# Kernel tuning notes

Hardware: AMD Instinct MI355X
Metric: run time of the kernel (lower is better)

The kernel has to match this reference:

```python
import jax, jax.numpy as jnp
import numpy as np

B, L, E, H = 2, 2048, 1024, 16
D = E // H

def setup_inputs() -> dict:
    key = jax.random.key(0)
    ks = jax.random.split(key, 6)
    values = jax.random.normal(ks[0], (B, L, E), dtype=jnp.float32)
    keys = jax.random.normal(ks[1], (B, L, E), dtype=jnp.float32)
    query = jax.random.normal(ks[2], (B, L, E), dtype=jnp.float32)
    mask = jax.random.randint(ks[3], (B, 1, L, L), 0, 2, dtype=jnp.int32)
    W_out = jax.random.normal(ks[4], (E, E), dtype=jnp.float32) * 0.02
    b_out = jax.random.normal(ks[5], (E,), dtype=jnp.float32) * 0.02
    return {"values": values, "keys": keys, "query": query, "mask": mask,
            "W_out": W_out, "b_out": b_out}

def reference(values, keys, query, mask, W_out, b_out):
    # Note: source module never applies its per-head q/k/v Linear layers;
    # it only reshapes inputs, so we do the same.
    b, l, e = query.shape
    v = values.reshape(b, l, H, D)   # [B, K, H, D]
    k = keys.reshape(b, l, H, D)     # [B, K, H, D]
    q = query.reshape(b, l, H, D)    # [B, Q, H, D]
    # scores[b,h,q,k] = sum_d q[b,q,h,d] * k[b,k,h,d]
    scores = jnp.einsum('bqhd,bkhd->bhqk', q, k)
    scores = jnp.where(mask == 0, jnp.float32(-1e20), scores)
    # source scales by 1/sqrt(embed_size), not head_dim
    attn = jax.nn.softmax(scores / jnp.float32(E ** 0.5), axis=3)
    out = jnp.einsum('bhqk,bkhd->bqhd', attn, v).reshape(b, l, e)
    out = out @ W_out.T + b_out  # torch Linear: x @ W^T + b
    return out
```

## Files before the change

### kernel.cpp

```cpp
#include <hip/hip_runtime.h>
#include <hip/hip_bf16.h>

typedef __bf16 bf16;
typedef __bf16 bf16x8 __attribute__((ext_vector_type(8)));
typedef __bf16 bf16x4 __attribute__((ext_vector_type(4)));
typedef float  f32x4  __attribute__((ext_vector_type(4)));

#define B_ 2
#define L_ 2048
#define E_ 1024
#define H_ 16
#define D_ 64

__device__ __forceinline__ int swz(int r, int c) {
    return r * 64 + (((c ^ (r & 7)) & 7) << 3);
}

__global__ __launch_bounds__(256) void cvt_bf16_kernel(const float* __restrict__ in,
                                                       bf16* __restrict__ out, int n4, float scale) {
    int i = blockIdx.x * blockDim.x + threadIdx.x;
    int stride = gridDim.x * blockDim.x;
    for (; i < n4; i += stride) {
        float4 f = reinterpret_cast<const float4*>(in)[i];
        bf16x4 o;
        o.x = (bf16)(f.x * scale); o.y = (bf16)(f.y * scale);
        o.z = (bf16)(f.z * scale); o.w = (bf16)(f.w * scale);
        reinterpret_cast<bf16x4*>(out)[i] = o;
    }
}

__global__ __launch_bounds__(256) void vtrans_kernel(const float* __restrict__ v,
                                                     bf16* __restrict__ vt) {
    __shared__ __attribute__((aligned(16))) bf16 tile[64 * 72];
    int bh = blockIdx.y;
    int b = bh >> 4, h = bh & 15;
    int k0 = blockIdx.x * 64;
    int t = threadIdx.x;
    int kk = t >> 2, d0 = (t & 3) * 16;
    const float* src = v + (((size_t)(b * L_ + k0 + kk)) * H_ + h) * D_ + d0;
    float4 f[4];
#pragma unroll
    for (int i = 0; i < 4; i++) f[i] = reinterpret_cast<const float4*>(src)[i];
#pragma unroll
    for (int i = 0; i < 16; i++) {
        float val = reinterpret_cast<const float*>(f)[i];
        tile[(d0 + i) * 72 + kk] = (bf16)val;
    }
    __syncthreads();
    int dd = t >> 2, c = (t & 3) * 16;
    bf16* dst = vt + ((size_t)bh * 64 + dd) * 2048 + k0 + c;
    *reinterpret_cast<uint4*>(dst)     = *reinterpret_cast<const uint4*>(&tile[dd * 72 + c]);
    *reinterpret_cast<uint4*>(dst + 8) = *reinterpret_cast<const uint4*>(&tile[dd * 72 + c + 8]);
}

__global__ __launch_bounds__(256) void mtrans_kernel(const int* __restrict__ mask,
                                                     unsigned short* __restrict__ mt) {
    __shared__ __attribute__((aligned(16))) unsigned char tile[64 * 80];
    int b = blockIdx.z;
    int q0 = blockIdx.x * 64, k0 = blockIdx.y * 64;
    int t = threadIdx.x;
    int qq = t >> 2, kc = (t & 3) * 16;
    const int* src = mask + (size_t)b * L_ * L_ + (size_t)(q0 + qq) * L_ + k0 + kc;
    int4 m[4];
#pragma unroll
    for (int i = 0; i < 4; i++) m[i] = reinterpret_cast<const int4*>(src)[i];
#pragma unroll
    for (int i = 0; i < 16; i++)
        tile[(kc + i) * 80 + qq] = (unsigned char)reinterpret_cast<const int*>(m)[i];
    __syncthreads();
    int kk = t >> 2, q16 = (t & 3) * 16;
    unsigned int v = 0;
#pragma unroll
    for (int i = 0; i < 16; i++)
        v |= ((unsigned int)(tile[kk * 80 + q16 + i] & 1)) << i;
    mt[((size_t)(b * L_) + k0 + kk) * (L_ / 16) + (q0 >> 4) + (t & 3)] = (unsigned short)v;
}

__global__ __launch_bounds__(256, 4) void attn_kernel(const bf16* __restrict__ qb,
                                                      const bf16* __restrict__ kb,
                                                      const bf16* __restrict__ vt,
                                                      const unsigned int* __restrict__ mt,
                                                      bf16* __restrict__ xb) {
    __shared__ __attribute__((aligned(16))) bf16 Qs[64 * 64];
    __shared__ __attribute__((aligned(16))) bf16 Ks[64 * 64];
    __shared__ __attribute__((aligned(16))) bf16 Vs[64 * 64];
    __shared__ __attribute__((aligned(16))) bf16 Ps[4][16 * 72];
    __shared__ unsigned int Ms32[64 * 2];

    const int bh = blockIdx.y, b = bh >> 4, h = bh & 15;
    const int q0 = blockIdx.x * 64;
    const int t = threadIdx.x;
    const int w = t >> 6, lane = t & 63, quad = lane >> 4, ln = lane & 15;
    const int r_ = t >> 2, c2 = (t & 3) * 2;

    {
        const bf16* src = qb + (((size_t)(b * L_ + q0 + r_)) * H_ + h) * D_ + c2 * 8;
        *reinterpret_cast<uint4*>(&Qs[swz(r_, c2)])     = *reinterpret_cast<const uint4*>(src);
        *reinterpret_cast<uint4*>(&Qs[swz(r_, c2 + 1)]) = *reinterpret_cast<const uint4*>(src + 8);
    }
    __syncthreads();

    bf16x8 aq[2];
#pragma unroll
    for (int dc = 0; dc < 2; dc++)
        aq[dc] = *reinterpret_cast<const bf16x8*>(&Qs[swz(w * 16 + ln, dc * 4 + quad)]);

    f32x4 o[4], lf;
    const f32x4 zero = {0.f, 0.f, 0.f, 0.f};
    lf = zero;
#pragma unroll
    for (int di = 0; di < 4; di++) o[di] = zero;
    bf16x8 ones;
#pragma unroll
    for (int i = 0; i < 8; i++) ones[i] = (bf16)1.0f;

    const int mshift = (w & 1) * 16 + quad * 4;
    const int mword = (w >> 1);

    for (int kt = 0; kt < L_ / 64; kt++) {
        const int k0 = kt * 64;
        {
            const bf16* ksrc = kb + (((size_t)(b * L_ + k0 + r_)) * H_ + h) * D_ + c2 * 8;
            *reinterpret_cast<uint4*>(&Ks[swz(r_, c2)])     = *reinterpret_cast<const uint4*>(ksrc);
            *reinterpret_cast<uint4*>(&Ks[swz(r_, c2 + 1)]) = *reinterpret_cast<const uint4*>(ksrc + 8);
            const bf16* vsrc = vt + ((size_t)bh * 64 + r_) * 2048 + k0 + c2 * 8;
            *reinterpret_cast<uint4*>(&Vs[swz(r_, c2)])     = *reinterpret_cast<const uint4*>(vsrc);
            *reinterpret_cast<uint4*>(&Vs[swz(r_, c2 + 1)]) = *reinterpret_cast<const uint4*>(vsrc + 8);
            if (t < 128) {
                int k = t >> 1, half = t & 1;
                Ms32[k * 2 + half] = mt[((size_t)(b * L_) + k0 + k) * (L_ / 32) + (q0 >> 5) + half];
            }
        }
        __syncthreads();

        f32x4 s[4];
#pragma unroll
        for (int ni = 0; ni < 4; ni++) s[ni] = zero;
#pragma unroll
        for (int ni = 0; ni < 4; ni++) {
#pragma unroll
            for (int dc = 0; dc < 2; dc++) {
                bf16x8 bk = *reinterpret_cast<const bf16x8*>(&Ks[swz(ni * 16 + ln, dc * 4 + quad)]);
                s[ni] = __builtin_amdgcn_mfma_f32_16x16x32_bf16(aq[dc], bk, s[ni], 0, 0, 0);
            }
        }

#pragma unroll
        for (int ni = 0; ni < 4; ni++) {
            unsigned int mw = Ms32[(ni * 16 + ln) * 2 + mword];
#pragma unroll
            for (int r = 0; r < 4; r++) {
                float p = __builtin_amdgcn_exp2f(s[ni][r]) *
                          (float)((mw >> (mshift + r)) & 1u);
                Ps[w][(quad * 4 + r) * 72 + ni * 16 + ln] = (bf16)p;
            }
        }

        bf16x8 ap[2];
#pragma unroll
        for (int kc = 0; kc < 2; kc++)
            ap[kc] = *reinterpret_cast<const bf16x8*>(&Ps[w][ln * 72 + (kc * 4 + quad) * 8]);
#pragma unroll
        for (int di = 0; di < 4; di++) {
#pragma unroll
            for (int kc = 0; kc < 2; kc++) {
                bf16x8 bv = *reinterpret_cast<const bf16x8*>(&Vs[swz(di * 16 + ln, kc * 4 + quad)]);
                o[di] = __builtin_amdgcn_mfma_f32_16x16x32_bf16(ap[kc], bv, o[di], 0, 0, 0);
            }
        }
#pragma unroll
        for (int kc = 0; kc < 2; kc++)
            lf = __builtin_amdgcn_mfma_f32_16x16x32_bf16(ap[kc], ones, lf, 0, 0, 0);
        __syncthreads();
    }

#pragma unroll
    for (int r = 0; r < 4; r++) {
        float rinv = 1.0f / lf[r];
        int q = w * 16 + quad * 4 + r;
#pragma unroll
        for (int di = 0; di < 4; di++) {
            xb[((size_t)(b * L_ + q0 + q)) * E_ + h * 64 + di * 16 + ln] =
                (bf16)(o[di][r] * rinv);
        }
    }
}

__global__ __launch_bounds__(256, 4) void proj_kernel(const bf16* __restrict__ xb,
                                                      const bf16* __restrict__ wb,
                                                      const float* __restrict__ bias,
                                                      float* __restrict__ out) {
    __shared__ __attribute__((aligned(16))) bf16 As[64 * 64];
    __shared__ __attribute__((aligned(16))) bf16 Bs[64 * 64];
    const int n0 = blockIdx.x * 64, m0 = blockIdx.y * 64;
    const int t = threadIdx.x;
    const int w = t >> 6, lane = t & 63, quad = lane >> 4, ln = lane & 15;
    const int wm = w >> 1, wn = w & 1;
    const int r_ = t >> 2, c2 = (t & 3) * 2;

    f32x4 c[2][2];
    const f32x4 zero = {0.f, 0.f, 0.f, 0.f};
#pragma unroll
    for (int mi = 0; mi < 2; mi++)
#pragma unroll
        for (int ni = 0; ni < 2; ni++) c[mi][ni] = zero;

    for (int kt = 0; kt < E_ / 64; kt++) {
        const int k0 = kt * 64;
        {
            const bf16* asrc = xb + (size_t)(m0 + r_) * E_ + k0 + c2 * 8;
            const bf16* bsrc = wb + (size_t)(n0 + r_) * E_ + k0 + c2 * 8;
            *reinterpret_cast<uint4*>(&As[swz(r_, c2)])     = *reinterpret_cast<const uint4*>(asrc);
            *reinterpret_cast<uint4*>(&As[swz(r_, c2 + 1)]) = *reinterpret_cast<const uint4*>(asrc + 8);
            *reinterpret_cast<uint4*>(&Bs[swz(r_, c2)])     = *reinterpret_cast<const uint4*>(bsrc);
            *reinterpret_cast<uint4*>(&Bs[swz(r_, c2 + 1)]) = *reinterpret_cast<const uint4*>(bsrc + 8);
        }
        __syncthreads();
#pragma unroll
        for (int kc = 0; kc < 2; kc++) {
            bf16x8 a[2], bb[2];
#pragma unroll
            for (int mi = 0; mi < 2; mi++)
                a[mi] = *reinterpret_cast<const bf16x8*>(&As[swz(wm * 32 + mi * 16 + ln, kc * 4 + quad)]);
#pragma unroll
            for (int ni = 0; ni < 2; ni++)
                bb[ni] = *reinterpret_cast<const bf16x8*>(&Bs[swz(wn * 32 + ni * 16 + ln, kc * 4 + quad)]);
#pragma unroll
            for (int mi = 0; mi < 2; mi++)
#pragma unroll
                for (int ni = 0; ni < 2; ni++)
                    c[mi][ni] = __builtin_amdgcn_mfma_f32_16x16x32_bf16(a[mi], bb[ni], c[mi][ni], 0, 0, 0);
        }
        __syncthreads();
    }
#pragma unroll
    for (int ni = 0; ni < 2; ni++) {
        float bv = bias[n0 + wn * 32 + ni * 16 + ln];
#pragma unroll
        for (int mi = 0; mi < 2; mi++)
#pragma unroll
            for (int r = 0; r < 4; r++) {
                int row = m0 + wm * 32 + mi * 16 + quad * 4 + r;
                int col = n0 + wn * 32 + ni * 16 + ln;
                out[(size_t)row * E_ + col] = c[mi][ni][r] + bv;
            }
    }
}

extern "C" void kernel_launch(void* const* d_in, const int* in_sizes, int n_in,
                              void* d_out, int out_size, void* d_ws, size_t ws_size,
                              hipStream_t stream) {
    (void)in_sizes; (void)n_in; (void)out_size; (void)ws_size;
    const float* values = (const float*)d_in[0];
    const float* keys   = (const float*)d_in[1];
    const float* query  = (const float*)d_in[2];
    const int*   mask   = (const int*)d_in[3];
    const float* W_out  = (const float*)d_in[4];
    const float* b_out  = (const float*)d_in[5];
    float* out = (float*)d_out;

    char* ws = (char*)d_ws;
    bf16* qb = (bf16*)(ws);
    bf16* kb = (bf16*)(ws + 8388608);
    bf16* vt = (bf16*)(ws + 16777216);
    bf16* wb = (bf16*)(ws + 25165824);
    unsigned short* mt = (unsigned short*)(ws + 27262976);
    bf16* xb = (bf16*)(ws + 35651584);

    const float CSCALE = 1.4426950408889634f / 32.0f;

    cvt_bf16_kernel<<<1024, 256, 0, stream>>>(query, qb, (B_ * L_ * E_) / 4, CSCALE);
    cvt_bf16_kernel<<<1024, 256, 0, stream>>>(keys,  kb, (B_ * L_ * E_) / 4, 1.0f);
    cvt_bf16_kernel<<<64, 256, 0, stream>>>(W_out, wb, (E_ * E_) / 4, 1.0f);
    vtrans_kernel<<<dim3(L_ / 64, B_ * H_), 256, 0, stream>>>(values, vt);
    mtrans_kernel<<<dim3(L_ / 64, L_ / 64, B_), 256, 0, stream>>>(mask, mt);
    attn_kernel<<<dim3(L_ / 64, B_ * H_), 256, 0, stream>>>(qb, kb, vt, (const unsigned int*)mt, xb);
    proj_kernel<<<dim3(E_ / 64, (B_ * L_) / 64), 256, 0, stream>>>(xb, wb, b_out, out);
}
```

Baseline: 228.8 us.

## Fuse Q/K conversion into attention, merge prep kernels, split warps over keys

Removes the separate Q and K fp32-to-bf16 conversion kernels; the attention kernel now loads fp32 Q/K and converts while staging to shared memory. The V transpose, mask bit-packing and weight conversion are merged into one prep kernel launch. Attention warps are rearranged into a 2x2 grid over query and key halves, so each warp reuses K/V fragments for two query tiles, with a shared-memory reduction of partial outputs and row sums at the end. This trades extra fp32 K reads per query block for fewer launches and less workspace traffic.

```diff
diff --git a/kernel.cpp b/kernel.cpp
--- a/kernel.cpp
+++ b/kernel.cpp
@@ -16,116 +16,139 @@
     return r * 64 + (((c ^ (r & 7)) & 7) << 3);
 }
 
-__global__ __launch_bounds__(256) void cvt_bf16_kernel(const float* __restrict__ in,
-                                                       bf16* __restrict__ out, int n4, float scale) {
-    int i = blockIdx.x * blockDim.x + threadIdx.x;
-    int stride = gridDim.x * blockDim.x;
-    for (; i < n4; i += stride) {
-        float4 f = reinterpret_cast<const float4*>(in)[i];
-        bf16x4 o;
-        o.x = (bf16)(f.x * scale); o.y = (bf16)(f.y * scale);
-        o.z = (bf16)(f.z * scale); o.w = (bf16)(f.w * scale);
-        reinterpret_cast<bf16x4*>(out)[i] = o;
-    }
-}
-
-__global__ __launch_bounds__(256) void vtrans_kernel(const float* __restrict__ v,
-                                                     bf16* __restrict__ vt) {
-    __shared__ __attribute__((aligned(16))) bf16 tile[64 * 72];
-    int bh = blockIdx.y;
-    int b = bh >> 4, h = bh & 15;
-    int k0 = blockIdx.x * 64;
-    int t = threadIdx.x;
-    int kk = t >> 2, d0 = (t & 3) * 16;
-    const float* src = v + (((size_t)(b * L_ + k0 + kk)) * H_ + h) * D_ + d0;
-    float4 f[4];
-#pragma unroll
-    for (int i = 0; i < 4; i++) f[i] = reinterpret_cast<const float4*>(src)[i];
-#pragma unroll
-    for (int i = 0; i < 16; i++) {
-        float val = reinterpret_cast<const float*>(f)[i];
-        tile[(d0 + i) * 72 + kk] = (bf16)val;
-    }
-    __syncthreads();
-    int dd = t >> 2, c = (t & 3) * 16;
-    bf16* dst = vt + ((size_t)bh * 64 + dd) * 2048 + k0 + c;
-    *reinterpret_cast<uint4*>(dst)     = *reinterpret_cast<const uint4*>(&tile[dd * 72 + c]);
-    *reinterpret_cast<uint4*>(dst + 8) = *reinterpret_cast<const uint4*>(&tile[dd * 72 + c + 8]);
-}
-
-__global__ __launch_bounds__(256) void mtrans_kernel(const int* __restrict__ mask,
-                                                     unsigned short* __restrict__ mt) {
-    __shared__ __attribute__((aligned(16))) unsigned char tile[64 * 80];
-    int b = blockIdx.z;
-    int q0 = blockIdx.x * 64, k0 = blockIdx.y * 64;
-    int t = threadIdx.x;
-    int qq = t >> 2, kc = (t & 3) * 16;
-    const int* src = mask + (size_t)b * L_ * L_ + (size_t)(q0 + qq) * L_ + k0 + kc;
-    int4 m[4];
-#pragma unroll
-    for (int i = 0; i < 4; i++) m[i] = reinterpret_cast<const int4*>(src)[i];
-#pragma unroll
-    for (int i = 0; i < 16; i++)
-        tile[(kc + i) * 80 + qq] = (unsigned char)reinterpret_cast<const int*>(m)[i];
-    __syncthreads();
-    int kk = t >> 2, q16 = (t & 3) * 16;
-    unsigned int v = 0;
-#pragma unroll
-    for (int i = 0; i < 16; i++)
-        v |= ((unsigned int)(tile[kk * 80 + q16 + i] & 1)) << i;
-    mt[((size_t)(b * L_) + k0 + kk) * (L_ / 16) + (q0 >> 4) + (t & 3)] = (unsigned short)v;
-}
-
-__global__ __launch_bounds__(256, 4) void attn_kernel(const bf16* __restrict__ qb,
-                                                      const bf16* __restrict__ kb,
+__global__ __launch_bounds__(256) void prep_kernel(const float* __restrict__ v,
+                                                   const int* __restrict__ mask,
+                                                   const float* __restrict__ W,
+                                                   bf16* __restrict__ vt,
+                                                   unsigned short* __restrict__ mt,
+                                                   bf16* __restrict__ wb) {
+    __shared__ __attribute__((aligned(16))) char sbuf[9216];
+    const int bid = blockIdx.x;
+    const int t = threadIdx.x;
+    if (bid < 1024) {
+        bf16* tile = (bf16*)sbuf;
+        int bh = bid >> 5, b = bh >> 4, h = bh & 15;
+        int k0 = (bid & 31) * 64;
+        int kk = t >> 2, d0 = (t & 3) * 16;
+        const float* src = v + (((size_t)(b * L_ + k0 + kk)) * H_ + h) * D_ + d0;
+        float4 f[4];
+#pragma unroll
+        for (int i = 0; i < 4; i++) f[i] = reinterpret_cast<const float4*>(src)[i];
+#pragma unroll
+        for (int i = 0; i < 16; i++) {
+            float val = reinterpret_cast<const float*>(f)[i];
+            tile[(d0 + i) * 72 + kk] = (bf16)val;
+        }
+        __syncthreads();
+        int dd = t >> 2, c = (t & 3) * 16;
+        bf16* dst = vt + ((size_t)bh * 64 + dd) * 2048 + k0 + c;
+        *reinterpret_cast<uint4*>(dst)     = *reinterpret_cast<const uint4*>(&tile[dd * 72 + c]);
+        *reinterpret_cast<uint4*>(dst + 8) = *reinterpret_cast<const uint4*>(&tile[dd * 72 + c + 8]);
+    } else if (bid < 3072) {
+        unsigned char* tile = (unsigned char*)sbuf;
+        int idx = bid - 1024;
+        int b = idx >> 10, k0 = ((idx >> 5) & 31) * 64, q0 = (idx & 31) * 64;
+        int qq = t >> 2, kc = (t & 3) * 16;
+        const int* src = mask + (size_t)b * L_ * L_ + (size_t)(q0 + qq) * L_ + k0 + kc;
+        int4 m[4];
+#pragma unroll
+        for (int i = 0; i < 4; i++) m[i] = reinterpret_cast<const int4*>(src)[i];
+#pragma unroll
+        for (int i = 0; i < 16; i++)
+            tile[(kc + i) * 80 + qq] = (unsigned char)reinterpret_cast<const int*>(m)[i];
+        __syncthreads();
+        int kk = t >> 2, q16 = (t & 3) * 16;
+        unsigned int bits = 0;
+#pragma unroll
+        for (int i = 0; i < 16; i++)
+            bits |= ((unsigned int)(tile[kk * 80 + q16 + i] & 1)) << i;
+        mt[((size_t)(b * L_) + k0 + kk) * (L_ / 16) + (q0 >> 4) + (t & 3)] = (unsigned short)bits;
+    } else {
+        int widx = bid - 3072;
+#pragma unroll
+        for (int j = 0; j < 16; j++) {
+            int i = widx * 4096 + j * 256 + t;
+            float4 f = reinterpret_cast<const float4*>(W)[i];
+            bf16x4 o;
+            o.x = (bf16)f.x; o.y = (bf16)f.y; o.z = (bf16)f.z; o.w = (bf16)f.w;
+            reinterpret_cast<bf16x4*>(wb)[i] = o;
+        }
+    }
+}
+
+__global__ __launch_bounds__(256, 4) void attn_kernel(const float* __restrict__ q_,
+                                                      const float* __restrict__ k_,
                                                       const bf16* __restrict__ vt,
                                                       const unsigned int* __restrict__ mt,
                                                       bf16* __restrict__ xb) {
-    __shared__ __attribute__((aligned(16))) bf16 Qs[64 * 64];
-    __shared__ __attribute__((aligned(16))) bf16 Ks[64 * 64];
-    __shared__ __attribute__((aligned(16))) bf16 Vs[64 * 64];
-    __shared__ __attribute__((aligned(16))) bf16 Ps[4][16 * 72];
-    __shared__ unsigned int Ms32[64 * 2];
+    __shared__ __attribute__((aligned(16))) char smem[27136];
+    bf16* Ks = (bf16*)smem;
+    bf16* Vs = (bf16*)(smem + 8192);
+    bf16* Ps = (bf16*)(smem + 16384);
+    bf16* Qs = (bf16*)(smem + 16384);
+    unsigned int* Ms32 = (unsigned int*)(smem + 26624);
+    float* Om = (float*)smem;
 
     const int bh = blockIdx.y, b = bh >> 4, h = bh & 15;
     const int q0 = blockIdx.x * 64;
     const int t = threadIdx.x;
     const int w = t >> 6, lane = t & 63, quad = lane >> 4, ln = lane & 15;
-    const int r_ = t >> 2, c2 = (t & 3) * 2;
+    const int wq = w & 1, wk = w >> 1;
+    const int r_ = t >> 2, cc = t & 3;
+
+    const float CSCALE = 1.4426950408889634f / 32.0f;
 
     {
-        const bf16* src = qb + (((size_t)(b * L_ + q0 + r_)) * H_ + h) * D_ + c2 * 8;
-        *reinterpret_cast<uint4*>(&Qs[swz(r_, c2)])     = *reinterpret_cast<const uint4*>(src);
-        *reinterpret_cast<uint4*>(&Qs[swz(r_, c2 + 1)]) = *reinterpret_cast<const uint4*>(src + 8);
+        const float* src = q_ + (((size_t)(b * L_ + q0 + r_)) * H_ + h) * D_ + cc * 16;
+        float4 f[4];
+#pragma unroll
+        for (int i = 0; i < 4; i++) f[i] = reinterpret_cast<const float4*>(src)[i];
+        bf16 tmp[16];
+#pragma unroll
+        for (int i = 0; i < 16; i++)
+            tmp[i] = (bf16)(reinterpret_cast<const float*>(f)[i] * CSCALE);
+        *reinterpret_cast<uint4*>(&Qs[swz(r_, cc * 2)])     = *reinterpret_cast<const uint4*>(&tmp[0]);
+        *reinterpret_cast<uint4*>(&Qs[swz(r_, cc * 2 + 1)]) = *reinterpret_cast<const uint4*>(&tmp[8]);
     }
     __syncthreads();
 
-    bf16x8 aq[2];
-#pragma unroll
-    for (int dc = 0; dc < 2; dc++)
-        aq[dc] = *reinterpret_cast<const bf16x8*>(&Qs[swz(w * 16 + ln, dc * 4 + quad)]);
-
-    f32x4 o[4], lf;
+    bf16x8 aq[2][2];
+#pragma unroll
+    for (int mi = 0; mi < 2; mi++)
+#pragma unroll
+        for (int dc = 0; dc < 2; dc++)
+            aq[mi][dc] = *reinterpret_cast<const bf16x8*>(&Qs[swz(wq * 32 + mi * 16 + ln, dc * 4 + quad)]);
+
+    f32x4 o[2][4], lf[2];
     const f32x4 zero = {0.f, 0.f, 0.f, 0.f};
-    lf = zero;
-#pragma unroll
-    for (int di = 0; di < 4; di++) o[di] = zero;
+#pragma unroll
+    for (int mi = 0; mi < 2; mi++) {
+        lf[mi] = zero;
+#pragma unroll
+        for (int di = 0; di < 4; di++) o[mi][di] = zero;
+    }
     bf16x8 ones;
 #pragma unroll
     for (int i = 0; i < 8; i++) ones[i] = (bf16)1.0f;
 
-    const int mshift = (w & 1) * 16 + quad * 4;
-    const int mword = (w >> 1);
+    bf16* Pw = Ps + w * 1280;
 
     for (int kt = 0; kt < L_ / 64; kt++) {
         const int k0 = kt * 64;
         {
-            const bf16* ksrc = kb + (((size_t)(b * L_ + k0 + r_)) * H_ + h) * D_ + c2 * 8;
-            *reinterpret_cast<uint4*>(&Ks[swz(r_, c2)])     = *reinterpret_cast<const uint4*>(ksrc);
-            *reinterpret_cast<uint4*>(&Ks[swz(r_, c2 + 1)]) = *reinterpret_cast<const uint4*>(ksrc + 8);
-            const bf16* vsrc = vt + ((size_t)bh * 64 + r_) * 2048 + k0 + c2 * 8;
-            *reinterpret_cast<uint4*>(&Vs[swz(r_, c2)])     = *reinterpret_cast<const uint4*>(vsrc);
-            *reinterpret_cast<uint4*>(&Vs[swz(r_, c2 + 1)]) = *reinterpret_cast<const uint4*>(vsrc + 8);
+            const float* ksrc = k_ + (((size_t)(b * L_ + k0 + r_)) * H_ + h) * D_ + cc * 16;
+            float4 f[4];
+#pragma unroll
+            for (int i = 0; i < 4; i++) f[i] = reinterpret_cast<const float4*>(ksrc)[i];
+            bf16 tmp[16];
+#pragma unroll
+            for (int i = 0; i < 16; i++)
+                tmp[i] = (bf16)reinterpret_cast<const float*>(f)[i];
+            *reinterpret_cast<uint4*>(&Ks[swz(r_, cc * 2)])     = *reinterpret_cast<const uint4*>(&tmp[0]);
+            *reinterpret_cast<uint4*>(&Ks[swz(r_, cc * 2 + 1)]) = *reinterpret_cast<const uint4*>(&tmp[8]);
+            const bf16* vsrc = vt + ((size_t)bh * 64 + r_) * 2048 + k0 + cc * 16;
+            *reinterpret_cast<uint4*>(&Vs[swz(r_, cc * 2)])     = *reinterpret_cast<const uint4*>(vsrc);
+            *reinterpret_cast<uint4*>(&Vs[swz(r_, cc * 2 + 1)]) = *reinterpret_cast<const uint4*>(vsrc + 8);
             if (t < 128) {
                 int k = t >> 1, half = t & 1;
                 Ms32[k * 2 + half] = mt[((size_t)(b * L_) + k0 + k) * (L_ / 32) + (q0 >> 5) + half];
@@ -133,55 +156,83 @@
         }
         __syncthreads();
 
-        f32x4 s[4];
-#pragma unroll
-        for (int ni = 0; ni < 4; ni++) s[ni] = zero;
-#pragma unroll
-        for (int ni = 0; ni < 4; ni++) {
+        f32x4 s[2][2];
+#pragma unroll
+        for (int mi = 0; mi < 2; mi++)
+#pragma unroll
+            for (int ni = 0; ni < 2; ni++) s[mi][ni] = zero;
+#pragma unroll
+        for (int ni = 0; ni < 2; ni++) {
 #pragma unroll
             for (int dc = 0; dc < 2; dc++) {
-                bf16x8 bk = *reinterpret_cast<const bf16x8*>(&Ks[swz(ni * 16 + ln, dc * 4 + quad)]);
-                s[ni] = __builtin_amdgcn_mfma_f32_16x16x32_bf16(aq[dc], bk, s[ni], 0, 0, 0);
+                bf16x8 bk = *reinterpret_cast<const bf16x8*>(&Ks[swz(wk * 32 + ni * 16 + ln, dc * 4 + quad)]);
+#pragma unroll
+                for (int mi = 0; mi < 2; mi++)
+                    s[mi][ni] = __builtin_amdgcn_mfma_f32_16x16x32_bf16(aq[mi][dc], bk, s[mi][ni], 0, 0, 0);
             }
         }
 
 #pragma unroll
-        for (int ni = 0; ni < 4; ni++) {
-            unsigned int mw = Ms32[(ni * 16 + ln) * 2 + mword];
-#pragma unroll
-            for (int r = 0; r < 4; r++) {
-                float p = __builtin_amdgcn_exp2f(s[ni][r]) *
-                          (float)((mw >> (mshift + r)) & 1u);
-                Ps[w][(quad * 4 + r) * 72 + ni * 16 + ln] = (bf16)p;
+        for (int ni = 0; ni < 2; ni++) {
+            unsigned int mw = Ms32[(wk * 32 + ni * 16 + ln) * 2 + wq];
+#pragma unroll
+            for (int mi = 0; mi < 2; mi++) {
+#pragma unroll
+                for (int r = 0; r < 4; r++) {
+                    float p = __builtin_amdgcn_exp2f(s[mi][ni][r]) *
+                              (float)((mw >> (mi * 16 + quad * 4 + r)) & 1u);
+                    Pw[(mi * 16 + quad * 4 + r) * 40 + ni * 16 + ln] = (bf16)p;
+                }
             }
         }
 
         bf16x8 ap[2];
 #pragma unroll
-        for (int kc = 0; kc < 2; kc++)
-            ap[kc] = *reinterpret_cast<const bf16x8*>(&Ps[w][ln * 72 + (kc * 4 + quad) * 8]);
+        for (int mi = 0; mi < 2; mi++)
+            ap[mi] = *reinterpret_cast<const bf16x8*>(&Pw[(mi * 16 + ln) * 40 + quad * 8]);
 #pragma unroll
         for (int di = 0; di < 4; di++) {
-#pragma unroll
-            for (int kc = 0; kc < 2; kc++) {
-                bf16x8 bv = *reinterpret_cast<const bf16x8*>(&Vs[swz(di * 16 + ln, kc * 4 + quad)]);
-                o[di] = __builtin_amdgcn_mfma_f32_16x16x32_bf16(ap[kc], bv, o[di], 0, 0, 0);
-            }
-        }
-#pragma unroll
-        for (int kc = 0; kc < 2; kc++)
-            lf = __builtin_amdgcn_mfma_f32_16x16x32_bf16(ap[kc], ones, lf, 0, 0, 0);
-        __syncthreads();
-    }
-
-#pragma unroll
-    for (int r = 0; r < 4; r++) {
-        float rinv = 1.0f / lf[r];
-        int q = w * 16 + quad * 4 + r;
-#pragma unroll
-        for (int di = 0; di < 4; di++) {
-            xb[((size_t)(b * L_ + q0 + q)) * E_ + h * 64 + di * 16 + ln] =
-                (bf16)(o[di][r] * rinv);
+            bf16x8 bv = *reinterpret_cast<const bf16x8*>(&Vs[swz(di * 16 + ln, wk * 4 + quad)]);
+#pragma unroll
+            for (int mi = 0; mi < 2; mi++)
+                o[mi][di] = __builtin_amdgcn_mfma_f32_16x16x32_bf16(ap[mi], bv, o[mi][di], 0, 0, 0);
+        }
+#pragma unroll
+        for (int mi = 0; mi < 2; mi++)
+            lf[mi] = __builtin_amdgcn_mfma_f32_16x16x32_bf16(ap[mi], ones, lf[mi], 0, 0, 0);
+        __syncthreads();
+    }
+
+    if (wk == 1) {
+#pragma unroll
+        for (int mi = 0; mi < 2; mi++) {
+#pragma unroll
+            for (int di = 0; di < 4; di++)
+#pragma unroll
+                for (int r = 0; r < 4; r++)
+                    Om[(wq * 32 + mi * 16 + quad * 4 + r) * 68 + di * 16 + ln] = o[mi][di][r];
+            if (ln == 0)
+#pragma unroll
+                for (int r = 0; r < 4; r++)
+                    Om[(wq * 32 + mi * 16 + quad * 4 + r) * 68 + 64] = lf[mi][r];
+        }
+    }
+    __syncthreads();
+    if (wk == 0) {
+#pragma unroll
+        for (int mi = 0; mi < 2; mi++) {
+            float lt[4];
+#pragma unroll
+            for (int r = 0; r < 4; r++)
+                lt[r] = 1.0f / (lf[mi][r] + Om[(wq * 32 + mi * 16 + quad * 4 + r) * 68 + 64]);
+#pragma unroll
+            for (int di = 0; di < 4; di++)
+#pragma unroll
+                for (int r = 0; r < 4; r++) {
+                    int q = wq * 32 + mi * 16 + quad * 4 + r;
+                    float val = (o[mi][di][r] + Om[q * 68 + di * 16 + ln]) * lt[r];
+                    xb[((size_t)(b * L_ + q0 + q)) * E_ + h * 64 + di * 16 + ln] = (bf16)val;
+                }
         }
     }
 }
@@ -196,7 +247,7 @@
     const int t = threadIdx.x;
     const int w = t >> 6, lane = t & 63, quad = lane >> 4, ln = lane & 15;
     const int wm = w >> 1, wn = w & 1;
-    const int r_ = t >> 2, c2 = (t & 3) * 2;
+    const int r_ = t >> 1, c2 = (t & 1) * 4;
 
     f32x4 c[2][2];
     const f32x4 zero = {0.f, 0.f, 0.f, 0.f};
@@ -208,12 +259,13 @@
     for (int kt = 0; kt < E_ / 64; kt++) {
         const int k0 = kt * 64;
         {
-            const bf16* asrc = xb + (size_t)(m0 + r_) * E_ + k0 + c2 * 8;
-            const bf16* bsrc = wb + (size_t)(n0 + r_) * E_ + k0 + c2 * 8;
-            *reinterpret_cast<uint4*>(&As[swz(r_, c2)])     = *reinterpret_cast<const uint4*>(asrc);
-            *reinterpret_cast<uint4*>(&As[swz(r_, c2 + 1)]) = *reinterpret_cast<const uint4*>(asrc + 8);
-            *reinterpret_cast<uint4*>(&Bs[swz(r_, c2)])     = *reinterpret_cast<const uint4*>(bsrc);
-            *reinterpret_cast<uint4*>(&Bs[swz(r_, c2 + 1)]) = *reinterpret_cast<const uint4*>(bsrc + 8);
+            const bf16* asrc = xb + (size_t)(m0 + (t >> 2)) * E_ + k0 + (t & 3) * 16;
+            const bf16* bsrc = wb + (size_t)(n0 + (t >> 2)) * E_ + k0 + (t & 3) * 16;
+            int rr = t >> 2, c4 = (t & 3) * 2;
+            *reinterpret_cast<uint4*>(&As[swz(rr, c4)])     = *reinterpret_cast<const uint4*>(asrc);
+            *reinterpret_cast<uint4*>(&As[swz(rr, c4 + 1)]) = *reinterpret_cast<const uint4*>(asrc + 8);
+            *reinterpret_cast<uint4*>(&Bs[swz(rr, c4)])     = *reinterpret_cast<const uint4*>(bsrc);
+            *reinterpret_cast<uint4*>(&Bs[swz(rr, c4 + 1)]) = *reinterpret_cast<const uint4*>(bsrc + 8);
         }
         __syncthreads();
 #pragma unroll
@@ -260,20 +312,12 @@
     float* out = (float*)d_out;
 
     char* ws = (char*)d_ws;
-    bf16* qb = (bf16*)(ws);
-    bf16* kb = (bf16*)(ws + 8388608);
-    bf16* vt = (bf16*)(ws + 16777216);
-    bf16* wb = (bf16*)(ws + 25165824);
-    unsigned short* mt = (unsigned short*)(ws + 27262976);
-    bf16* xb = (bf16*)(ws + 35651584);
-
-    const float CSCALE = 1.4426950408889634f / 32.0f;
-
-    cvt_bf16_kernel<<<1024, 256, 0, stream>>>(query, qb, (B_ * L_ * E_) / 4, CSCALE);
-    cvt_bf16_kernel<<<1024, 256, 0, stream>>>(keys,  kb, (B_ * L_ * E_) / 4, 1.0f);
-    cvt_bf16_kernel<<<64, 256, 0, stream>>>(W_out, wb, (E_ * E_) / 4, 1.0f);
-    vtrans_kernel<<<dim3(L_ / 64, B_ * H_), 256, 0, stream>>>(values, vt);
-    mtrans_kernel<<<dim3(L_ / 64, L_ / 64, B_), 256, 0, stream>>>(mask, mt);
-    attn_kernel<<<dim3(L_ / 64, B_ * H_), 256, 0, stream>>>(qb, kb, vt, (const unsigned int*)mt, xb);
+    bf16* vt = (bf16*)(ws);
+    bf16* wb = (bf16*)(ws + 8388608);
+    unsigned short* mt = (unsigned short*)(ws + 10485760);
+    bf16* xb = (bf16*)(ws + 11534336);
+
+    prep_kernel<<<3136, 256, 0, stream>>>(values, mask, W_out, vt, mt, wb);
+    attn_kernel<<<dim3(L_ / 64, B_ * H_), 256, 0, stream>>>(query, keys, vt, (const unsigned int*)mt, xb);
     proj_kernel<<<dim3(E_ / 64, (B_ * L_) / 64), 256, 0, stream>>>(xb, wb, b_out, out);
 }
```

Result: faster. 218.1 us (-4.7%).
